# Kernel tuning notes

Hardware: AMD Instinct MI355X
Metric: run time of the kernel (lower is better)

## Reference

```python
import jax, jax.numpy as jnp
import numpy as np

NEG_SLOPE = 0.2

def setup_inputs() -> dict:
    key = jax.random.key(0)
    k1, k2, k3, k4 = jax.random.split(key, 4)
    B, N, Fin, H, Fo = 8, 2000, 128, 4, 64
    x = jax.random.normal(k1, (B, N, Fin), dtype=jnp.float32)
    adj = jax.random.randint(k2, (N, N), 0, 2, dtype=jnp.int32)
    W = jax.random.normal(k3, (Fin, H * Fo), dtype=jnp.float32) * (1.0 / np.sqrt(Fin))
    a = jax.random.normal(k4, (H, 2 * Fo), dtype=jnp.float32) * 0.1
    return {"x": x, "adj": adj, "W": W, "a": a}

def reference(x, adj, W, a):
    B, N, _ = x.shape
    H, F2 = a.shape
    Fo = F2 // 2
    h = (x @ W).reshape(B, N, H, Fo)  # [B,N,H,Fo]
    # cat([h_i,h_j])*a summed over 2Fo decomposes into per-node src/dst scores
    a_src, a_dst = a[:, :Fo], a[:, Fo:]
    e_i = jnp.einsum('bnhf,hf->bnh', h, a_src)  # source (query) contribution
    e_j = jnp.einsum('bnhf,hf->bnh', h, a_dst)  # target (key) contribution
    e = jax.nn.leaky_relu(e_i[:, :, None, :] + e_j[:, None, :, :], NEG_SLOPE)  # [B,N,N,H]
    mask = (adj == 0)[None, :, :, None]
    e = jnp.where(mask, -jnp.inf, e)
    alpha = jax.nn.softmax(e, axis=2)  # softmax over neighbors j
    # dropout is identity in eval mode
    out = jnp.einsum('bijh,bjhf->bihf', alpha, h).mean(axis=2)  # [B,N,Fo]
    return out, alpha
```

## Files before the change

kernel.cpp:

```cpp
#include <hip/hip_runtime.h>
#include <math.h>

#define BB 8
#define NN 2000
#define FIN 128
#define HH 4
#define FO 64
#define CC 256

typedef short bf16x8 __attribute__((ext_vector_type(8)));
typedef float f32x4 __attribute__((ext_vector_type(4)));
typedef unsigned long long u64;

__device__ __forceinline__ unsigned short f2bf(float v) {
    union { float f; unsigned u; } x;
    x.f = v;
    unsigned r = x.u + 0x7fffu + ((x.u >> 16) & 1u);
    return (unsigned short)(r >> 16);
}

__global__ __launch_bounds__(256) void k_adjpad(const int* __restrict__ adj,
                                                u64* __restrict__ adjb,
                                                unsigned short* __restrict__ hT) {
    if (blockIdx.x < 1000) {
        const int lane = threadIdx.x & 63;
        for (int w = blockIdx.x * 4 + (threadIdx.x >> 6); w < 64000; w += 4000) {
            const int i = w >> 5, wd = w & 31;
            const int j = wd * 64 + lane;
            int av = 0;
            if (j < NN) av = adj[(size_t)i * NN + j];
            const u64 mask = __ballot(av != 0);
            if (lane == 0) adjb[(size_t)i * 32 + wd] = mask;
        }
    } else {
        const int k = (blockIdx.x - 1000) * 256 + threadIdx.x;
        const int bh = k / 384;
        const int r = k - bh * 384;
        const int ft = r / 96;
        const int c = r - ft * 96;
        size_t off;
        if (c < 32) off = 62 * 2048 + ft * 512 + 256 + c * 8;
        else        off = 63 * 2048 + ft * 512 + (size_t)(c - 32) * 8;
        uint4 z; z.x = 0; z.y = 0; z.z = 0; z.w = 0;
        *(uint4*)(hT + (size_t)bh * 131072 + off) = z;
    }
}

__global__ __launch_bounds__(256) void k_gemm_fused(const float* __restrict__ x,
                                                    const float* __restrict__ W,
                                                    const float* __restrict__ a,
                                                    float* __restrict__ e_src,
                                                    float* __restrict__ e_dst,
                                                    unsigned short* __restrict__ hT) {
    __shared__ __align__(16) char smraw[8192];
    float* xs = (float*)smraw;
    unsigned short* sm = (unsigned short*)smraw;
    const int row0 = blockIdx.x * 16;
    const int t = threadIdx.x;
    for (int k = t; k < 16 * FIN; k += 256) xs[k] = x[row0 * FIN + k];
    __syncthreads();
    const int c = t;
    const int h = c >> 6, f = c & 63, lane = t & 63;
    float acc[16];
#pragma unroll
    for (int r = 0; r < 16; ++r) acc[r] = 0.f;
#pragma unroll 2
    for (int k = 0; k < FIN; k += 4) {
        const float w0 = W[(k + 0) * CC + c];
        const float w1 = W[(k + 1) * CC + c];
        const float w2 = W[(k + 2) * CC + c];
        const float w3 = W[(k + 3) * CC + c];
#pragma unroll
        for (int r = 0; r < 16; ++r) {
            const float4 xv = *(const float4*)(xs + r * FIN + k);
            acc[r] = fmaf(xv.x, w0, fmaf(xv.y, w1, fmaf(xv.z, w2, fmaf(xv.w, w3, acc[r]))));
        }
    }
    const int b = row0 / NN;
    const int n0 = row0 - b * NN;
    const float aS = a[h * 2 * FO + f];
    const float aD = a[h * 2 * FO + FO + f];
#pragma unroll
    for (int r = 0; r < 16; ++r) {
        float p1 = acc[r] * aS;
        float p2 = acc[r] * aD;
#pragma unroll
        for (int off = 32; off > 0; off >>= 1) {
            p1 += __shfl_xor(p1, off);
            p2 += __shfl_xor(p2, off);
        }
        if (lane == 0) {
            e_src[(b * HH + h) * NN + n0 + r] = p1;
            e_dst[(b * HH + h) * NN + n0 + r] = p2;
        }
    }
    __syncthreads();
#pragma unroll
    for (int r = 0; r < 16; ++r) sm[r * 256 + c] = f2bf(acc[r]);
    __syncthreads();
    const int s = n0 >> 5;
    const int qbase = (n0 >> 3) & 3;
    unsigned short* base = hT + (size_t)b * HH * 131072 + s * 2048;
#pragma unroll
    for (int it2 = 0; it2 < 2; ++it2) {
        const int k2 = it2 * 256 + t;
        const int hh = (k2 >> 7) & 3, ft2 = (k2 >> 5) & 3, l16 = (k2 >> 1) & 15, g = k2 & 1;
        const int col = hh * 64 + ft2 * 16 + l16;
        unsigned v[4];
#pragma unroll
        for (int p = 0; p < 4; ++p) {
            const unsigned lo = sm[(g * 8 + 2 * p) * 256 + col];
            const unsigned hi = sm[(g * 8 + 2 * p + 1) * 256 + col];
            v[p] = lo | (hi << 16);
        }
        uint4 pkt; pkt.x = v[0]; pkt.y = v[1]; pkt.z = v[2]; pkt.w = v[3];
        *(uint4*)(base + (size_t)hh * 131072 + ft2 * 512 + (qbase + g) * 128 + l16 * 8) = pkt;
    }
}

__global__ __launch_bounds__(256) void k_out_mfma5(const u64* __restrict__ adjb,
                                                   const unsigned short* __restrict__ hT,
                                                   const float* __restrict__ e_src,
                                                   const float* __restrict__ e_dst,
                                                   float* __restrict__ rlArr,
                                                   float* __restrict__ out) {
    __shared__ __align__(16) float eds[HH][2048];
    const int blk = blockIdx.x;
    const int b = blk & 7;
    const int it = blk >> 3;
    const int i0 = it * 16;
    const int t = threadIdx.x;
    const int h = t >> 6, lane = t & 63;
    const int l16 = lane & 15, quad = lane >> 4;
    for (int idx = t; idx < 2048; idx += 256) {
        const int h2 = idx >> 9, j4 = (idx & 511) * 4;
        float4 v = {0.f, 0.f, 0.f, 0.f};
        if (j4 < NN) v = *(const float4*)(e_dst + (b * HH + h2) * NN + j4);
        *(float4*)(&eds[h2][j4]) = v;
    }
    __syncthreads();
    const int i = i0 + l16;
    const int bh = b * HH + h;
    const float es = e_src[bh * NN + i];
    const u64* ab = adjb + (size_t)i * 32;
    const unsigned short* hbase = hT + (size_t)bh * 131072 + (size_t)lane * 8;

    f32x4 acc[4];
#pragma unroll
    for (int ft = 0; ft < 4; ++ft) {
        acc[ft][0] = 0.f; acc[ft][1] = 0.f; acc[ft][2] = 0.f; acc[ft][3] = 0.f;
    }
    float psum = 0.f;

#pragma unroll 2
    for (int jt = 0; jt < 32; ++jt) {
        const u64 bits = ab[jt];
        const unsigned m0 = ((unsigned)(bits >> (quad * 8))) & 0xffu;
        const unsigned m1 = ((unsigned)(bits >> 32) >> (quad * 8)) & 0xffu;
        const float* ep = &eds[h][jt * 64 + quad * 8];
        const f32x4 ea0 = *(const f32x4*)(ep);
        const f32x4 ea1 = *(const f32x4*)(ep + 4);
        const f32x4 eb0 = *(const f32x4*)(ep + 32);
        const f32x4 eb1 = *(const f32x4*)(ep + 36);
        const unsigned short* hp0 = hbase + (size_t)jt * 4096;

        {
            const float ev[8] = {ea0[0], ea0[1], ea0[2], ea0[3], ea1[0], ea1[1], ea1[2], ea1[3]};
            bf16x8 bfr;
#pragma unroll
            for (int e = 0; e < 8; ++e) {
                float s = es + ev[e];
                s = s > 0.f ? s : 0.2f * s;
                float p = ((m0 >> e) & 1u) ? __expf(s) : 0.f;
                psum += p;
                bfr[e] = (short)f2bf(p);
            }
#pragma unroll
            for (int ft = 0; ft < 4; ++ft) {
                const bf16x8 af = *(const bf16x8*)(hp0 + ft * 512);
                acc[ft] = __builtin_amdgcn_mfma_f32_16x16x32_bf16(af, bfr, acc[ft], 0, 0, 0);
            }
        }
        {
            const float ev[8] = {eb0[0], eb0[1], eb0[2], eb0[3], eb1[0], eb1[1], eb1[2], eb1[3]};
            bf16x8 bfr;
#pragma unroll
            for (int e = 0; e < 8; ++e) {
                float s = es + ev[e];
                s = s > 0.f ? s : 0.2f * s;
                float p = ((m1 >> e) & 1u) ? __expf(s) : 0.f;
                psum += p;
                bfr[e] = (short)f2bf(p);
            }
#pragma unroll
            for (int ft = 0; ft < 4; ++ft) {
                const bf16x8 af = *(const bf16x8*)(hp0 + 2048 + ft * 512);
                acc[ft] = __builtin_amdgcn_mfma_f32_16x16x32_bf16(af, bfr, acc[ft], 0, 0, 0);
            }
        }
    }
    psum += __shfl_xor(psum, 16);
    psum += __shfl_xor(psum, 32);
    const float rl = 1.f / psum;
#pragma unroll
    for (int ft = 0; ft < 4; ++ft)
#pragma unroll
        for (int r = 0; r < 4; ++r) acc[ft][r] *= rl;
    if (quad == 0) rlArr[bh * NN + i] = rl;

    __syncthreads();
    float* red = (float*)eds;
#pragma unroll
    for (int ph = 0; ph < HH; ++ph) {
        if (h == ph) {
            if (ph == 0) {
#pragma unroll
                for (int ft = 0; ft < 4; ++ft)
                    *(f32x4*)(&red[l16 * 68 + ft * 16 + quad * 4]) = acc[ft];
            } else {
#pragma unroll
                for (int ft = 0; ft < 4; ++ft) {
                    f32x4 cur = *(const f32x4*)(&red[l16 * 68 + ft * 16 + quad * 4]);
#pragma unroll
                    for (int r = 0; r < 4; ++r) cur[r] += acc[ft][r];
                    *(f32x4*)(&red[l16 * 68 + ft * 16 + quad * 4]) = cur;
                }
            }
        }
        __syncthreads();
    }
    const int ii = t >> 4, f4 = (t & 15) * 4;
    const f32x4 v = *(const f32x4*)(&red[ii * 68 + f4]);
    f32x4 o;
#pragma unroll
    for (int r = 0; r < 4; ++r) o[r] = 0.25f * v[r];
    *(f32x4*)(out + (size_t)(b * NN + i0 + ii) * FO + f4) = o;
}

__global__ __launch_bounds__(256) void k_alpha_bits(const u64* __restrict__ adjb,
                                                    const float* __restrict__ e_src,
                                                    const float* __restrict__ e_dst,
                                                    const float* __restrict__ rlArr,
                                                    float* __restrict__ alpha) {
    const int bi = blockIdx.x;
    const int b = bi / NN, i = bi - b * NN;
    const int t = threadIdx.x;
    float ei[HH], rr[HH];
#pragma unroll
    for (int h = 0; h < HH; ++h) {
        ei[h] = e_src[(b * HH + h) * NN + i];
        rr[h] = rlArr[(b * HH + h) * NN + i];
    }
    const float* ed = e_dst + b * HH * NN;
    const u64* ab = adjb + (size_t)i * 32;
    float* arow = alpha + (size_t)(b * NN + i) * (NN * HH);
#pragma unroll
    for (int k = 0; k < 8; ++k) {
        const int j = k * 256 + t;
        if (j < NN) {
            const u64 wbits = ab[j >> 6];
            const bool av = (wbits >> (j & 63)) & 1ull;
            float o[HH];
#pragma unroll
            for (int h = 0; h < HH; ++h) {
                float s = ei[h] + ed[h * NN + j];
                s = s > 0.f ? s : 0.2f * s;
                o[h] = av ? __expf(s) * rr[h] : 0.f;
            }
            float4 ov = {o[0], o[1], o[2], o[3]};
            *(float4*)(arow + (size_t)j * HH) = ov;
        }
    }
}

__global__ __launch_bounds__(256) void k_alpha_adj(const int* __restrict__ adj,
                                                   const float* __restrict__ e_src,
                                                   const float* __restrict__ e_dst,
                                                   const float* __restrict__ rlArr,
                                                   float* __restrict__ alpha) {
    const int bi = blockIdx.x;
    const int b = bi / NN, i = bi - b * NN;
    const int t = threadIdx.x;
    float ei[HH], rr[HH];
#pragma unroll
    for (int h = 0; h < HH; ++h) {
        ei[h] = e_src[(b * HH + h) * NN + i];
        rr[h] = rlArr[(b * HH + h) * NN + i];
    }
    const float* ed = e_dst + b * HH * NN;
    const int* adjrow = adj + (size_t)i * NN;
    float* arow = alpha + (size_t)(b * NN + i) * (NN * HH);
#pragma unroll
    for (int k = 0; k < 8; ++k) {
        const int j = k * 256 + t;
        if (j < NN) {
            const bool av = adjrow[j] != 0;
            float o[HH];
#pragma unroll
            for (int h = 0; h < HH; ++h) {
                float s = ei[h] + ed[h * NN + j];
                s = s > 0.f ? s : 0.2f * s;
                o[h] = av ? __expf(s) * rr[h] : 0.f;
            }
            float4 ov = {o[0], o[1], o[2], o[3]};
            *(float4*)(arow + (size_t)j * HH) = ov;
        }
    }
}

extern "C" void kernel_launch(void* const* d_in, const int* in_sizes, int n_in,
                              void* d_out, int out_size, void* d_ws, size_t ws_size,
                              hipStream_t stream) {
    const float* x  = (const float*)d_in[0];
    const int* adj  = (const int*)d_in[1];
    const float* W  = (const float*)d_in[2];
    const float* a  = (const float*)d_in[3];

    float* out = (float*)d_out;
    float* alpha = out + (size_t)BB * NN * FO;

    unsigned short* hT = (unsigned short*)alpha;
    u64* adjb_scratch = (u64*)((char*)alpha + 8388608);

    char* ws = (char*)d_ws;
    float* e_src = (float*)ws;
    float* e_dst = (float*)(ws + 256000);
    float* rlArr = (float*)(ws + 512000);
    const bool ws_has_adjb = ws_size >= 1280000;
    u64* adjb = ws_has_adjb ? (u64*)(ws + 768000) : adjb_scratch;

    k_adjpad<<<1048, 256, 0, stream>>>(adj, adjb, hT);
    k_gemm_fused<<<1000, 256, 0, stream>>>(x, W, a, e_src, e_dst, hT);
    k_out_mfma5<<<1000, 256, 0, stream>>>(adjb, hT, e_src, e_dst, rlArr, out);
    if (ws_has_adjb)
        k_alpha_bits<<<16000, 256, 0, stream>>>(adjb, e_src, e_dst, rlArr, alpha);
    else
        k_alpha_adj<<<16000, 256, 0, stream>>>(adj, e_src, e_dst, rlArr, alpha);
}
```

Baseline: 641.2 us.

## Fuse alpha writes into attention MFMA kernel with two-pass softmax normalization

The adjacency bitpacking and hT padding kernel is merged into the GEMM launch as extra blocks. The attention kernel now makes a first pass to compute the softmax denominator, then a second pass that forms normalized probabilities, feeds them to the MFMA and stages them in shared memory. From there they are written straight to alpha, so the separate 16000-block alpha kernel is gone. Because hT aliases the start of the alpha buffer, rows that would overwrite hT (batch 0, first 288 rows) are deferred to a small tail kernel reading raw adj. This costs recomputing exp twice, a per-tile __syncthreads, and e_dst read from global instead of LDS.

After: 666.6 us. 4.0% more time.

```diff
diff --git a/kernel.cpp b/kernel.cpp
--- a/kernel.cpp
+++ b/kernel.cpp
@@ -19,44 +19,45 @@
     return (unsigned short)(r >> 16);
 }
 
-__global__ __launch_bounds__(256) void k_adjpad(const int* __restrict__ adj,
-                                                u64* __restrict__ adjb,
-                                                unsigned short* __restrict__ hT) {
-    if (blockIdx.x < 1000) {
-        const int lane = threadIdx.x & 63;
-        for (int w = blockIdx.x * 4 + (threadIdx.x >> 6); w < 64000; w += 4000) {
-            const int i = w >> 5, wd = w & 31;
-            const int j = wd * 64 + lane;
-            int av = 0;
-            if (j < NN) av = adj[(size_t)i * NN + j];
-            const u64 mask = __ballot(av != 0);
-            if (lane == 0) adjb[(size_t)i * 32 + wd] = mask;
-        }
-    } else {
-        const int k = (blockIdx.x - 1000) * 256 + threadIdx.x;
-        const int bh = k / 384;
-        const int r = k - bh * 384;
-        const int ft = r / 96;
-        const int c = r - ft * 96;
-        size_t off;
-        if (c < 32) off = 62 * 2048 + ft * 512 + 256 + c * 8;
-        else        off = 63 * 2048 + ft * 512 + (size_t)(c - 32) * 8;
-        uint4 z; z.x = 0; z.y = 0; z.z = 0; z.w = 0;
-        *(uint4*)(hT + (size_t)bh * 131072 + off) = z;
-    }
-}
-
-__global__ __launch_bounds__(256) void k_gemm_fused(const float* __restrict__ x,
-                                                    const float* __restrict__ W,
-                                                    const float* __restrict__ a,
-                                                    float* __restrict__ e_src,
-                                                    float* __restrict__ e_dst,
-                                                    unsigned short* __restrict__ hT) {
+__global__ __launch_bounds__(256) void k_gemm_all(const float* __restrict__ x,
+                                                  const float* __restrict__ W,
+                                                  const float* __restrict__ a,
+                                                  const int* __restrict__ adj,
+                                                  float* __restrict__ e_src,
+                                                  float* __restrict__ e_dst,
+                                                  unsigned short* __restrict__ hT,
+                                                  u64* __restrict__ adjb) {
+    const int t = threadIdx.x;
+    if (blockIdx.x >= 1000) {
+        const int bx = blockIdx.x - 1000;
+        if (bx < 1000) {
+            const int lane = t & 63;
+            for (int w = bx * 4 + (t >> 6); w < 64000; w += 4000) {
+                const int i = w >> 5, wd = w & 31;
+                const int j = wd * 64 + lane;
+                int av = 0;
+                if (j < NN) av = adj[(size_t)i * NN + j];
+                const u64 mask = __ballot(av != 0);
+                if (lane == 0) adjb[(size_t)i * 32 + wd] = mask;
+            }
+        } else {
+            const int k = (bx - 1000) * 256 + t;
+            const int bh = k / 384;
+            const int r = k - bh * 384;
+            const int ft = r / 96;
+            const int c = r - ft * 96;
+            size_t off;
+            if (c < 32) off = 62 * 2048 + ft * 512 + 256 + c * 8;
+            else        off = 63 * 2048 + ft * 512 + (size_t)(c - 32) * 8;
+            uint4 z; z.x = 0; z.y = 0; z.z = 0; z.w = 0;
+            *(uint4*)(hT + (size_t)bh * 131072 + off) = z;
+        }
+        return;
+    }
     __shared__ __align__(16) char smraw[8192];
     float* xs = (float*)smraw;
     unsigned short* sm = (unsigned short*)smraw;
     const int row0 = blockIdx.x * 16;
-    const int t = threadIdx.x;
     for (int k = t; k < 16 * FIN; k += 256) xs[k] = x[row0 * FIN + k];
     __syncthreads();
     const int c = t;
@@ -118,13 +119,14 @@
     }
 }
 
-__global__ __launch_bounds__(256) void k_out_mfma5(const u64* __restrict__ adjb,
+__global__ __launch_bounds__(256) void k_out_mfma6(const u64* __restrict__ adjb,
                                                    const unsigned short* __restrict__ hT,
                                                    const float* __restrict__ e_src,
                                                    const float* __restrict__ e_dst,
                                                    float* __restrict__ rlArr,
-                                                   float* __restrict__ out) {
-    __shared__ __align__(16) float eds[HH][2048];
+                                                   float* __restrict__ out,
+                                                   float* __restrict__ alpha) {
+    __shared__ __align__(16) float ps[2][16][HH][68];
     const int blk = blockIdx.x;
     const int b = blk & 7;
     const int it = blk >> 3;
@@ -132,49 +134,73 @@
     const int t = threadIdx.x;
     const int h = t >> 6, lane = t & 63;
     const int l16 = lane & 15, quad = lane >> 4;
-    for (int idx = t; idx < 2048; idx += 256) {
-        const int h2 = idx >> 9, j4 = (idx & 511) * 4;
-        float4 v = {0.f, 0.f, 0.f, 0.f};
-        if (j4 < NN) v = *(const float4*)(e_dst + (b * HH + h2) * NN + j4);
-        *(float4*)(&eds[h2][j4]) = v;
-    }
-    __syncthreads();
     const int i = i0 + l16;
     const int bh = b * HH + h;
     const float es = e_src[bh * NN + i];
+    const float* ed = e_dst + bh * NN;
     const u64* ab = adjb + (size_t)i * 32;
     const unsigned short* hbase = hT + (size_t)bh * 131072 + (size_t)lane * 8;
 
-    f32x4 acc[4];
-#pragma unroll
-    for (int ft = 0; ft < 4; ++ft) {
-        acc[ft][0] = 0.f; acc[ft][1] = 0.f; acc[ft][2] = 0.f; acc[ft][3] = 0.f;
-    }
     float psum = 0.f;
-
 #pragma unroll 2
     for (int jt = 0; jt < 32; ++jt) {
         const u64 bits = ab[jt];
         const unsigned m0 = ((unsigned)(bits >> (quad * 8))) & 0xffu;
         const unsigned m1 = ((unsigned)(bits >> 32) >> (quad * 8)) & 0xffu;
-        const float* ep = &eds[h][jt * 64 + quad * 8];
-        const f32x4 ea0 = *(const f32x4*)(ep);
-        const f32x4 ea1 = *(const f32x4*)(ep + 4);
-        const f32x4 eb0 = *(const f32x4*)(ep + 32);
-        const f32x4 eb1 = *(const f32x4*)(ep + 36);
+        const float* ep = ed + jt * 64 + quad * 8;
+        const float4 ea0 = *(const float4*)(ep);
+        const float4 ea1 = *(const float4*)(ep + 4);
+        const float4 eb0 = *(const float4*)(ep + 32);
+        const float4 eb1 = *(const float4*)(ep + 36);
+        const float ev0[8] = {ea0.x, ea0.y, ea0.z, ea0.w, ea1.x, ea1.y, ea1.z, ea1.w};
+        const float ev1[8] = {eb0.x, eb0.y, eb0.z, eb0.w, eb1.x, eb1.y, eb1.z, eb1.w};
+#pragma unroll
+        for (int e = 0; e < 8; ++e) {
+            float s0 = es + ev0[e]; s0 = s0 > 0.f ? s0 : 0.2f * s0;
+            float s1 = es + ev1[e]; s1 = s1 > 0.f ? s1 : 0.2f * s1;
+            psum += ((m0 >> e) & 1u) ? __expf(s0) : 0.f;
+            psum += ((m1 >> e) & 1u) ? __expf(s1) : 0.f;
+        }
+    }
+    psum += __shfl_xor(psum, 16);
+    psum += __shfl_xor(psum, 32);
+    const float rl = 1.f / psum;
+    if (quad == 0) rlArr[bh * NN + i] = rl;
+
+    f32x4 acc[4];
+#pragma unroll
+    for (int ft = 0; ft < 4; ++ft) {
+        acc[ft][0] = 0.f; acc[ft][1] = 0.f; acc[ft][2] = 0.f; acc[ft][3] = 0.f;
+    }
+    const bool wr = (b > 0) || (it >= 18);
+    const int ii = t >> 4, g = t & 15;
+    float* arowbase = alpha + ((size_t)b * NN + i0 + ii) * (NN * HH);
+    int buf = 0;
+    for (int jt = 0; jt < 32; ++jt) {
+        const u64 bits = ab[jt];
+        const unsigned m0 = ((unsigned)(bits >> (quad * 8))) & 0xffu;
+        const unsigned m1 = ((unsigned)(bits >> 32) >> (quad * 8)) & 0xffu;
+        const float* ep = ed + jt * 64 + quad * 8;
+        const float4 ea0 = *(const float4*)(ep);
+        const float4 ea1 = *(const float4*)(ep + 4);
+        const float4 eb0 = *(const float4*)(ep + 32);
+        const float4 eb1 = *(const float4*)(ep + 36);
+        const float ev0[8] = {ea0.x, ea0.y, ea0.z, ea0.w, ea1.x, ea1.y, ea1.z, ea1.w};
+        const float ev1[8] = {eb0.x, eb0.y, eb0.z, eb0.w, eb1.x, eb1.y, eb1.z, eb1.w};
         const unsigned short* hp0 = hbase + (size_t)jt * 4096;
-
         {
-            const float ev[8] = {ea0[0], ea0[1], ea0[2], ea0[3], ea1[0], ea1[1], ea1[2], ea1[3]};
+            f32x4 q0, q1;
             bf16x8 bfr;
 #pragma unroll
             for (int e = 0; e < 8; ++e) {
-                float s = es + ev[e];
+                float s = es + ev0[e];
                 s = s > 0.f ? s : 0.2f * s;
-                float p = ((m0 >> e) & 1u) ? __expf(s) : 0.f;
-                psum += p;
-                bfr[e] = (short)f2bf(p);
-            }
+                const float q = (((m0 >> e) & 1u) ? __expf(s) : 0.f) * rl;
+                bfr[e] = (short)f2bf(q);
+                if (e < 4) q0[e] = q; else q1[e - 4] = q;
+            }
+            *(f32x4*)(&ps[buf][l16][h][quad * 8]) = q0;
+            *(f32x4*)(&ps[buf][l16][h][quad * 8 + 4]) = q1;
 #pragma unroll
             for (int ft = 0; ft < 4; ++ft) {
                 const bf16x8 af = *(const bf16x8*)(hp0 + ft * 512);
@@ -182,34 +208,45 @@
             }
         }
         {
-            const float ev[8] = {eb0[0], eb0[1], eb0[2], eb0[3], eb1[0], eb1[1], eb1[2], eb1[3]};
+            f32x4 q0, q1;
             bf16x8 bfr;
 #pragma unroll
             for (int e = 0; e < 8; ++e) {
-                float s = es + ev[e];
+                float s = es + ev1[e];
                 s = s > 0.f ? s : 0.2f * s;
-                float p = ((m1 >> e) & 1u) ? __expf(s) : 0.f;
-                psum += p;
-                bfr[e] = (short)f2bf(p);
-            }
+                const float q = (((m1 >> e) & 1u) ? __expf(s) : 0.f) * rl;
+                bfr[e] = (short)f2bf(q);
+                if (e < 4) q0[e] = q; else q1[e - 4] = q;
+            }
+            *(f32x4*)(&ps[buf][l16][h][32 + quad * 8]) = q0;
+            *(f32x4*)(&ps[buf][l16][h][32 + quad * 8 + 4]) = q1;
 #pragma unroll
             for (int ft = 0; ft < 4; ++ft) {
                 const bf16x8 af = *(const bf16x8*)(hp0 + 2048 + ft * 512);
                 acc[ft] = __builtin_amdgcn_mfma_f32_16x16x32_bf16(af, bfr, acc[ft], 0, 0, 0);
             }
         }
-    }
-    psum += __shfl_xor(psum, 16);
-    psum += __shfl_xor(psum, 32);
-    const float rl = 1.f / psum;
-#pragma unroll
-    for (int ft = 0; ft < 4; ++ft)
-#pragma unroll
-        for (int r = 0; r < 4; ++r) acc[ft][r] *= rl;
-    if (quad == 0) rlArr[bh * NN + i] = rl;
-
+        __syncthreads();
+        if (wr) {
+            float* arow = arowbase + (size_t)jt * 256;
+            const int jlim = NN - jt * 64;
+#pragma unroll
+            for (int c = 0; c < 4; ++c) {
+                const int jl = c * 16 + g;
+                if (jl < jlim) {
+                    float4 ov;
+                    ov.x = ps[buf][ii][0][jl];
+                    ov.y = ps[buf][ii][1][jl];
+                    ov.z = ps[buf][ii][2][jl];
+                    ov.w = ps[buf][ii][3][jl];
+                    *(float4*)(arow + (size_t)jl * 4) = ov;
+                }
+            }
+        }
+        buf ^= 1;
+    }
     __syncthreads();
-    float* red = (float*)eds;
+    float* red = (float*)ps;
 #pragma unroll
     for (int ph = 0; ph < HH; ++ph) {
         if (h == ph) {
@@ -229,67 +266,29 @@
         }
         __syncthreads();
     }
-    const int ii = t >> 4, f4 = (t & 15) * 4;
-    const f32x4 v = *(const f32x4*)(&red[ii * 68 + f4]);
+    const int f4 = (t & 15) * 4;
+    const f32x4 v = *(const f32x4*)(&red[(t >> 4) * 68 + f4]);
     f32x4 o;
 #pragma unroll
     for (int r = 0; r < 4; ++r) o[r] = 0.25f * v[r];
-    *(f32x4*)(out + (size_t)(b * NN + i0 + ii) * FO + f4) = o;
-}
-
-__global__ __launch_bounds__(256) void k_alpha_bits(const u64* __restrict__ adjb,
+    *(f32x4*)(out + (size_t)(b * NN + i0 + (t >> 4)) * FO + f4) = o;
+}
+
+__global__ __launch_bounds__(256) void k_alpha_tail(const int* __restrict__ adj,
                                                     const float* __restrict__ e_src,
                                                     const float* __restrict__ e_dst,
                                                     const float* __restrict__ rlArr,
                                                     float* __restrict__ alpha) {
-    const int bi = blockIdx.x;
-    const int b = bi / NN, i = bi - b * NN;
+    const int i = blockIdx.x;
     const int t = threadIdx.x;
     float ei[HH], rr[HH];
 #pragma unroll
     for (int h = 0; h < HH; ++h) {
-        ei[h] = e_src[(b * HH + h) * NN + i];
-        rr[h] = rlArr[(b * HH + h) * NN + i];
-    }
-    const float* ed = e_dst + b * HH * NN;
-    const u64* ab = adjb + (size_t)i * 32;
-    float* arow = alpha + (size_t)(b * NN + i) * (NN * HH);
-#pragma unroll
-    for (int k = 0; k < 8; ++k) {
-        const int j = k * 256 + t;
-        if (j < NN) {
-            const u64 wbits = ab[j >> 6];
-            const bool av = (wbits >> (j & 63)) & 1ull;
-            float o[HH];
-#pragma unroll
-            for (int h = 0; h < HH; ++h) {
-                float s = ei[h] + ed[h * NN + j];
-                s = s > 0.f ? s : 0.2f * s;
-                o[h] = av ? __expf(s) * rr[h] : 0.f;
-            }
-            float4 ov = {o[0], o[1], o[2], o[3]};
-            *(float4*)(arow + (size_t)j * HH) = ov;
-        }
-    }
-}
-
-__global__ __launch_bounds__(256) void k_alpha_adj(const int* __restrict__ adj,
-                                                   const float* __restrict__ e_src,
-                                                   const float* __restrict__ e_dst,
-                                                   const float* __restrict__ rlArr,
-                                                   float* __restrict__ alpha) {
-    const int bi = blockIdx.x;
-    const int b = bi / NN, i = bi - b * NN;
-    const int t = threadIdx.x;
-    float ei[HH], rr[HH];
-#pragma unroll
-    for (int h = 0; h < HH; ++h) {
-        ei[h] = e_src[(b * HH + h) * NN + i];
-        rr[h] = rlArr[(b * HH + h) * NN + i];
-    }
-    const float* ed = e_dst + b * HH * NN;
+        ei[h] = e_src[h * NN + i];
+        rr[h] = rlArr[h * NN + i];
+    }
     const int* adjrow = adj + (size_t)i * NN;
-    float* arow = alpha + (size_t)(b * NN + i) * (NN * HH);
+    float* arow = alpha + (size_t)i * (NN * HH);
 #pragma unroll
     for (int k = 0; k < 8; ++k) {
         const int j = k * 256 + t;
@@ -298,7 +297,7 @@
             float o[HH];
 #pragma unroll
             for (int h = 0; h < HH; ++h) {
-                float s = ei[h] + ed[h * NN + j];
+                float s = ei[h] + e_dst[h * NN + j];
                 s = s > 0.f ? s : 0.2f * s;
                 o[h] = av ? __expf(s) * rr[h] : 0.f;
             }
@@ -329,11 +328,7 @@
     const bool ws_has_adjb = ws_size >= 1280000;
     u64* adjb = ws_has_adjb ? (u64*)(ws + 768000) : adjb_scratch;
 
-    k_adjpad<<<1048, 256, 0, stream>>>(adj, adjb, hT);
-    k_gemm_fused<<<1000, 256, 0, stream>>>(x, W, a, e_src, e_dst, hT);
-    k_out_mfma5<<<1000, 256, 0, stream>>>(adjb, hT, e_src, e_dst, rlArr, out);
-    if (ws_has_adjb)
-        k_alpha_bits<<<16000, 256, 0, stream>>>(adjb, e_src, e_dst, rlArr, alpha);
-    else
-        k_alpha_adj<<<16000, 256, 0, stream>>>(adj, e_src, e_dst, rlArr, alpha);
-}
+    k_gemm_all<<<2048, 256, 0, stream>>>(x, W, a, adj, e_src, e_dst, hT, adjb);
+    k_out_mfma6<<<1000, 256, 0, stream>>>(adjb, hT, e_src, e_dst, rlArr, out, alpha);
+    k_alpha_tail<<<288, 256, 0, stream>>>(adj, e_src, e_dst, rlArr, alpha);
+}
```
